# Kernel tuning notes

Hardware: AMD Instinct MI355X
Metric: run time of the kernel (lower is better)

The kernel has to match this reference:

```python
import jax, jax.numpy as jnp
import numpy as np

E = 16      # num experts
K = 2       # top-k
EPS = np.finfo(float).eps


def setup_inputs() -> dict:
    key = jax.random.key(0)
    k1, k2, k3 = jax.random.split(key, 3)
    B, D_IN, D_OUT = 16384, 1024, 512
    x = jax.random.normal(k1, (B, D_IN), dtype=jnp.float32)
    w_router = jax.random.normal(k2, (D_IN, E), dtype=jnp.float32) * 0.02
    w_experts = jax.random.normal(k3, (E, D_IN, D_OUT), dtype=jnp.float32) * 0.02
    return {"x": x, "w_router": w_router, "w_experts": w_experts}


def reference(x, w_router, w_experts):
    # --- noisy_top_k_gating (eval path: clean logits, no noise) ---
    logits = x @ w_router                      # [B, E]
    top_vals, top_idx = jax.lax.top_k(logits, K)   # [B, K]
    top_gates = jax.nn.softmax(top_vals, axis=1)   # softmax over top-k logits
    B = x.shape[0]
    gates = jnp.zeros_like(logits).at[jnp.arange(B)[:, None], top_idx].set(top_gates)  # [B, E]

    # --- per-expert encode (dense form; zero gates null out non-dispatched pairs,
    #     matching SparseDispatcher's sparse dispatch/combine math exactly) ---
    expert_out = jnp.einsum('bd,edh->beh', x, w_experts)  # [B, E, d_out]

    # --- SparseDispatcher.combine: exp -> gate-weight -> index_add -> eps clamp -> log ---
    combined = jnp.einsum('be,beh->bh', gates, jnp.exp(expert_out))  # [B, d_out]
    combined = jnp.where(combined == 0, jnp.asarray(EPS, combined.dtype), combined)
    return jnp.log(combined)
```

## Files before the change

### kernel.cpp

```cpp
#include <hip/hip_runtime.h>
#include <hip/hip_bf16.h>

typedef unsigned short u16_t;
typedef unsigned int   u32_t;

#define B_ROWS  16384
#define D_IN    1024
#define D_OUT   512
#define NEXP    16
#define CNT_STRIDE 16
#define EPSF    2.2204460492503131e-16f

using short8  = __attribute__((ext_vector_type(8))) short;
using floatx4 = __attribute__((ext_vector_type(4))) float;

__device__ __forceinline__ u16_t f2bf(float f) {
    u32_t u = __float_as_uint(f);
    u += 0x7fffu + ((u >> 16) & 1u);
    return (u16_t)(u >> 16);
}

__global__ __launch_bounds__(256) void transpose_wr(
        const float* __restrict__ wr, float* __restrict__ wrT) {
    int i = blockIdx.x * 256 + threadIdx.x;
    int e = i >> 10, d = i & 1023;
    wrT[i] = wr[d * NEXP + e];
}

__global__ __launch_bounds__(256) void convert_x(
        const float* __restrict__ x, u16_t* __restrict__ xb) {
    size_t i = ((size_t)blockIdx.x * 256 + threadIdx.x) * 8;
    float4 a = *(const float4*)(x + i);
    float4 b = *(const float4*)(x + i + 4);
    union { u16_t us[8]; uint4 v; } p;
    p.us[0] = f2bf(a.x); p.us[1] = f2bf(a.y); p.us[2] = f2bf(a.z); p.us[3] = f2bf(a.w);
    p.us[4] = f2bf(b.x); p.us[5] = f2bf(b.y); p.us[6] = f2bf(b.z); p.us[7] = f2bf(b.w);
    *(uint4*)(xb + i) = p.v;
}

__global__ __launch_bounds__(256) void convert_wT(
        const float* __restrict__ w, u16_t* __restrict__ wT) {
    int b = blockIdx.x;
    int e  = b >> 8;
    int k0 = ((b >> 1) & 127) * 8;
    int n  = (b & 1) * 256 + threadIdx.x;
    const float* src = w + ((size_t)e * D_IN + k0) * D_OUT + n;
    union { u16_t us[8]; uint4 v; } p;
    #pragma unroll
    for (int j = 0; j < 8; ++j) p.us[j] = f2bf(src[(size_t)j * D_OUT]);
    *(uint4*)(wT + ((size_t)e * D_OUT + n) * D_IN + k0) = p.v;
}

__global__ __launch_bounds__(256) void router_kernel(
        const float* __restrict__ x, const float* __restrict__ wrT,
        int* __restrict__ counts, int* __restrict__ rowlist,
        float* __restrict__ gatelist) {
    __shared__ float wsh[NEXP * D_IN];
    __shared__ int hist[NEXP], base[NEXP], hist2[NEXP];
    __shared__ unsigned char eidx_sh[32][2];
    __shared__ float g_sh[32][2];

    int t = threadIdx.x;
    {
        const float4* src = (const float4*)wrT;
        float4* dst = (float4*)wsh;
        #pragma unroll
        for (int i = 0; i < 16; ++i) dst[t + 256 * i] = src[t + 256 * i];
    }
    if (t < NEXP) { hist[t] = 0; hist2[t] = 0; }
    __syncthreads();

    int lr = t >> 3, q = t & 7;
    int row = blockIdx.x * 32 + lr;
    const float4* xq = (const float4*)(x + (size_t)row * D_IN + q * 128);

    double acc[NEXP];
    #pragma unroll
    for (int e = 0; e < NEXP; ++e) acc[e] = 0.0;

    for (int i = 0; i < 32; ++i) {
        int ii = (i + q * 4) & 31;
        float4 xv = xq[ii];
        double x0 = xv.x, x1 = xv.y, x2 = xv.z, x3 = xv.w;
        int d = q * 128 + ii * 4;
        #pragma unroll
        for (int e = 0; e < NEXP; ++e) {
            float4 wv = *(const float4*)(&wsh[e * D_IN + d]);
            acc[e] += x0 * (double)wv.x;
            acc[e] += x1 * (double)wv.y;
            acc[e] += x2 * (double)wv.z;
            acc[e] += x3 * (double)wv.w;
        }
    }
    #pragma unroll
    for (int e = 0; e < NEXP; ++e) {
        acc[e] += __shfl_xor(acc[e], 1);
        acc[e] += __shfl_xor(acc[e], 2);
        acc[e] += __shfl_xor(acc[e], 4);
    }
    if (q == 0) {
        int i1 = 0; double v1 = acc[0];
        #pragma unroll
        for (int e = 1; e < NEXP; ++e) if (acc[e] > v1) { v1 = acc[e]; i1 = e; }
        int i2 = -1; double v2 = -1.0e300;
        #pragma unroll
        for (int e = 0; e < NEXP; ++e) if (e != i1 && acc[e] > v2) { v2 = acc[e]; i2 = e; }
        double ed = exp(v2 - v1);
        double s = 1.0 + ed;
        eidx_sh[lr][0] = (unsigned char)i1; g_sh[lr][0] = (float)(1.0 / s);
        eidx_sh[lr][1] = (unsigned char)i2; g_sh[lr][1] = (float)(ed / s);
        atomicAdd(&hist[i1], 1);
        atomicAdd(&hist[i2], 1);
    }
    __syncthreads();
    if (t < NEXP) base[t] = atomicAdd(&counts[t * CNT_STRIDE], hist[t]);
    __syncthreads();
    if (t < 64) {
        int r = t >> 1, sl = t & 1;
        int e = eidx_sh[r][sl];
        int pos = base[e] + atomicAdd(&hist2[e], 1);
        rowlist[e * B_ROWS + pos] = ((blockIdx.x * 32 + r) << 1) | sl;
        gatelist[e * B_ROWS + pos] = g_sh[r][sl];
    }
}

template<bool USE_CONTRIB>
__global__ __launch_bounds__(256) void moe_gemm_bf16(
        const u16_t* __restrict__ xb, const u16_t* __restrict__ wT,
        const int* __restrict__ counts, const int* __restrict__ rowlist,
        const float* __restrict__ gatelist,
        float* __restrict__ out, float* __restrict__ contrib) {
    int e = blockIdx.z;
    int n_e = counts[e * CNT_STRIDE];
    int ty = blockIdx.y;
    if (ty * 128 >= n_e) return;
    int n0 = blockIdx.x * 128;

    __shared__ u16_t Ash[128][40];
    __shared__ u16_t Bsh[128][40];
    __shared__ int   rid_sh[128];
    __shared__ float gt_sh[128];

    int t = threadIdx.x;
    if (t < 128) {
        int gi = ty * 128 + t;
        int v = 0; float g = 0.f;
        if (gi < n_e) { v = rowlist[e * B_ROWS + gi]; g = gatelist[e * B_ROWS + gi]; }
        rid_sh[t] = v; gt_sh[t] = g;
    }
    __syncthreads();

    int hr = t >> 1, hh = t & 1;
    const u16_t* aptr = xb + (size_t)(rid_sh[hr] >> 1) * D_IN + hh * 16;
    const u16_t* bptr = wT + ((size_t)e * D_OUT + n0 + hr) * D_IN + hh * 16;

    int lane = t & 63, wv = t >> 6;
    int wm = wv >> 1, wn = wv & 1;
    int lm = lane & 15, q = lane >> 4;

    floatx4 acc[4][4];
    #pragma unroll
    for (int mi = 0; mi < 4; ++mi)
        #pragma unroll
        for (int ni = 0; ni < 4; ++ni)
            acc[mi][ni] = (floatx4){0.f, 0.f, 0.f, 0.f};

    for (int it = 0; it < D_IN / 32; ++it) {
        uint4 a0 = *(const uint4*)(aptr);
        uint4 a1 = *(const uint4*)(aptr + 8);
        uint4 b0 = *(const uint4*)(bptr);
        uint4 b1 = *(const uint4*)(bptr + 8);
        aptr += 32; bptr += 32;

        __syncthreads();
        *(uint4*)(&Ash[hr][hh * 16])     = a0;
        *(uint4*)(&Ash[hr][hh * 16 + 8]) = a1;
        *(uint4*)(&Bsh[hr][hh * 16])     = b0;
        *(uint4*)(&Bsh[hr][hh * 16 + 8]) = b1;
        __syncthreads();

        short8 afr[4];
        #pragma unroll
        for (int mi = 0; mi < 4; ++mi)
            afr[mi] = *(const short8*)(&Ash[wm * 64 + mi * 16 + lm][q * 8]);
        short8 bfr[4];
        #pragma unroll
        for (int ni = 0; ni < 4; ++ni)
            bfr[ni] = *(const short8*)(&Bsh[wn * 64 + ni * 16 + lm][q * 8]);
        #pragma unroll
        for (int mi = 0; mi < 4; ++mi)
            #pragma unroll
            for (int ni = 0; ni < 4; ++ni)
                acc[mi][ni] = __builtin_amdgcn_mfma_f32_16x16x32_bf16(
                    afr[mi], bfr[ni], acc[mi][ni], 0, 0, 0);
    }

    #pragma unroll
    for (int mi = 0; mi < 4; ++mi) {
        int rbase = wm * 64 + mi * 16 + q * 4;
        #pragma unroll
        for (int r = 0; r < 4; ++r) {
            int row = rbase + r;
            int gi = ty * 128 + row;
            bool ok = gi < n_e;
            int v = rid_sh[row];
            float g = gt_sh[row];
            size_t orow = (size_t)(v >> 1) * D_OUT;
            #pragma unroll
            for (int ni = 0; ni < 4; ++ni) {
                int c = n0 + wn * 64 + ni * 16 + lm;
                float val = g * __expf(acc[mi][ni][r]);
                if (ok) {
                    if (USE_CONTRIB) {
                        float* dst = (v & 1) ? contrib : out;
                        dst[orow + c] = val;
                    } else {
                        atomicAdd(&out[orow + c], val);
                    }
                }
            }
        }
    }
}

template<bool USE_CONTRIB>
__global__ __launch_bounds__(256) void moe_gemm(
        const float* __restrict__ x, const float* __restrict__ w,
        const int* __restrict__ counts, const int* __restrict__ rowlist,
        const float* __restrict__ gatelist,
        float* __restrict__ out, float* __restrict__ contrib) {
    int e = blockIdx.z;
    int n_e = counts[e * CNT_STRIDE];
    int ty = blockIdx.y;
    if (ty * 128 >= n_e) return;
    int n0 = blockIdx.x * 128;

    __shared__ u16_t Ash[128][40];
    __shared__ u32_t Bsh[16][132];
    __shared__ int   rid_sh[128];
    __shared__ float gt_sh[128];

    int t = threadIdx.x;
    if (t < 128) {
        int gi = ty * 128 + t;
        int v = 0; float g = 0.f;
        if (gi < n_e) { v = rowlist[e * B_ROWS + gi]; g = gatelist[e * B_ROWS + gi]; }
        rid_sh[t] = v; gt_sh[t] = g;
    }
    __syncthreads();

    int ar = t >> 1, ah = t & 1;
    const float* xptr = x + (size_t)(rid_sh[ar] >> 1) * D_IN + ah * 16;
    int bkp = t >> 4, bng = t & 15;
    const float* wptr = w + (size_t)e * (D_IN * D_OUT)
                          + (size_t)(2 * bkp) * D_OUT + n0 + bng * 8;

    int lane = t & 63, wv = t >> 6;
    int wm = wv >> 1, wn = wv & 1;
    int lm = lane & 15, q = lane >> 4;

    floatx4 acc[4][4];
    #pragma unroll
    for (int mi = 0; mi < 4; ++mi)
        #pragma unroll
        for (int ni = 0; ni < 4; ++ni)
            acc[mi][ni] = (floatx4){0.f, 0.f, 0.f, 0.f};

    for (int it = 0; it < D_IN / 32; ++it) {
        float4 av0 = *(const float4*)(xptr + 0);
        float4 av1 = *(const float4*)(xptr + 4);
        float4 av2 = *(const float4*)(xptr + 8);
        float4 av3 = *(const float4*)(xptr + 12);
        xptr += 32;
        float4 b0 = *(const float4*)(wptr + 0);
        float4 b1 = *(const float4*)(wptr + 4);
        float4 b2 = *(const float4*)(wptr + D_OUT);
        float4 b3 = *(const float4*)(wptr + D_OUT + 4);
        wptr += 32 * D_OUT;

        __syncthreads();
        {
            union { u16_t us[16]; uint4 v[2]; } ap;
            float af[16] = {av0.x, av0.y, av0.z, av0.w, av1.x, av1.y, av1.z, av1.w,
                            av2.x, av2.y, av2.z, av2.w, av3.x, av3.y, av3.z, av3.w};
            #pragma unroll
            for (int j = 0; j < 16; ++j) ap.us[j] = f2bf(af[j]);
            *(uint4*)(&Ash[ar][ah * 16])     = ap.v[0];
            *(uint4*)(&Ash[ar][ah * 16 + 8]) = ap.v[1];
        }
        {
            union { u32_t up[8]; uint4 v[2]; } bp;
            bp.up[0] = (u32_t)f2bf(b0.x) | ((u32_t)f2bf(b2.x) << 16);
            bp.up[1] = (u32_t)f2bf(b0.y) | ((u32_t)f2bf(b2.y) << 16);
            bp.up[2] = (u32_t)f2bf(b0.z) | ((u32_t)f2bf(b2.z) << 16);
            bp.up[3] = (u32_t)f2bf(b0.w) | ((u32_t)f2bf(b2.w) << 16);
            bp.up[4] = (u32_t)f2bf(b1.x) | ((u32_t)f2bf(b3.x) << 16);
            bp.up[5] = (u32_t)f2bf(b1.y) | ((u32_t)f2bf(b3.y) << 16);
            bp.up[6] = (u32_t)f2bf(b1.z) | ((u32_t)f2bf(b3.z) << 16);
            bp.up[7] = (u32_t)f2bf(b1.w) | ((u32_t)f2bf(b3.w) << 16);
            *(uint4*)(&Bsh[bkp][bng * 8])     = bp.v[0];
            *(uint4*)(&Bsh[bkp][bng * 8 + 4]) = bp.v[1];
        }
        __syncthreads();

        short8 afr[4];
        #pragma unroll
        for (int mi = 0; mi < 4; ++mi)
            afr[mi] = *(const short8*)(&Ash[wm * 64 + mi * 16 + lm][q * 8]);
        short8 bfr[4];
        #pragma unroll
        for (int ni = 0; ni < 4; ++ni) {
            int nn = wn * 64 + ni * 16 + lm;
            union { uint4 u; short8 s; } cv;
            cv.u.x = Bsh[q * 4 + 0][nn];
            cv.u.y = Bsh[q * 4 + 1][nn];
            cv.u.z = Bsh[q * 4 + 2][nn];
            cv.u.w = Bsh[q * 4 + 3][nn];
            bfr[ni] = cv.s;
        }
        #pragma unroll
        for (int mi = 0; mi < 4; ++mi)
            #pragma unroll
            for (int ni = 0; ni < 4; ++ni)
                acc[mi][ni] = __builtin_amdgcn_mfma_f32_16x16x32_bf16(
                    afr[mi], bfr[ni], acc[mi][ni], 0, 0, 0);
    }

    #pragma unroll
    for (int mi = 0; mi < 4; ++mi) {
        int rbase = wm * 64 + mi * 16 + q * 4;
        #pragma unroll
        for (int r = 0; r < 4; ++r) {
            int row = rbase + r;
            int gi = ty * 128 + row;
            bool ok = gi < n_e;
            int v = rid_sh[row];
            float g = gt_sh[row];
            size_t orow = (size_t)(v >> 1) * D_OUT;
            #pragma unroll
            for (int ni = 0; ni < 4; ++ni) {
                int c = n0 + wn * 64 + ni * 16 + lm;
                float val = g * __expf(acc[mi][ni][r]);
                if (ok) {
                    if (USE_CONTRIB) {
                        float* dst = (v & 1) ? contrib : out;
                        dst[orow + c] = val;
                    } else {
                        atomicAdd(&out[orow + c], val);
                    }
                }
            }
        }
    }
}

__global__ __launch_bounds__(256) void combine_add_log(
        float* __restrict__ out, const float* __restrict__ contrib, int n4) {
    int i = blockIdx.x * blockDim.x + threadIdx.x;
    if (i >= n4) return;
    float4 a = ((const float4*)out)[i];
    float4 b = ((const float4*)contrib)[i];
    float4 r;
    float s;
    s = a.x + b.x; s = (s == 0.f) ? EPSF : s; r.x = __logf(s);
    s = a.y + b.y; s = (s == 0.f) ? EPSF : s; r.y = __logf(s);
    s = a.z + b.z; s = (s == 0.f) ? EPSF : s; r.z = __logf(s);
    s = a.w + b.w; s = (s == 0.f) ? EPSF : s; r.w = __logf(s);
    ((float4*)out)[i] = r;
}

__global__ __launch_bounds__(256) void log_inplace(float* __restrict__ out, int n4) {
    int i = blockIdx.x * blockDim.x + threadIdx.x;
    if (i >= n4) return;
    float4 a = ((float4*)out)[i];
    float4 r;
    float s;
    s = a.x; s = (s == 0.f) ? EPSF : s; r.x = __logf(s);
    s = a.y; s = (s == 0.f) ? EPSF : s; r.y = __logf(s);
    s = a.z; s = (s == 0.f) ? EPSF : s; r.z = __logf(s);
    s = a.w; s = (s == 0.f) ? EPSF : s; r.w = __logf(s);
    ((float4*)out)[i] = r;
}

extern "C" void kernel_launch(void* const* d_in, const int* in_sizes, int n_in,
                              void* d_out, int out_size, void* d_ws, size_t ws_size,
                              hipStream_t stream) {
    const float* x  = (const float*)d_in[0];
    const float* wr = (const float*)d_in[1];
    const float* we = (const float*)d_in[2];
    float* out = (float*)d_out;
    char* ws = (char*)d_ws;

    size_t off = 0;
    int*   counts  = (int*)(ws + off);   off += 1024;
    int*   rowlist = (int*)(ws + off);   off += (size_t)NEXP * B_ROWS * 4;
    float* gates   = (float*)(ws + off); off += (size_t)NEXP * B_ROWS * 4;
    float* wrT     = (float*)(ws + off); off += (size_t)NEXP * D_IN * 4;
    float* contrib = (float*)(ws + off); off += (size_t)B_ROWS * D_OUT * 4;
    size_t tier2_need = off;
    u16_t* xb      = (u16_t*)(ws + off); off += (size_t)B_ROWS * D_IN * 2;
    u16_t* wTb     = (u16_t*)(ws + off); off += (size_t)NEXP * D_IN * D_OUT * 2;
    size_t tier3_need = off;

    hipMemsetAsync(counts, 0, 1024, stream);
    transpose_wr<<<NEXP * D_IN / 256, 256, 0, stream>>>(wr, wrT);
    router_kernel<<<B_ROWS / 32, 256, 0, stream>>>(x, wrT, counts, rowlist, gates);

    dim3 g(D_OUT / 128, B_ROWS / 128, NEXP);
    int n4 = B_ROWS * D_OUT / 4;

    if (ws_size >= tier3_need) {
        convert_x<<<(B_ROWS * D_IN / 8) / 256, 256, 0, stream>>>(x, xb);
        convert_wT<<<NEXP * 128 * 2, 256, 0, stream>>>(we, wTb);
        moe_gemm_bf16<true><<<g, 256, 0, stream>>>(xb, wTb, counts, rowlist, gates, out, contrib);
        combine_add_log<<<(n4 + 255) / 256, 256, 0, stream>>>(out, contrib, n4);
    } else if (ws_size >= tier2_need) {
        moe_gemm<true><<<g, 256, 0, stream>>>(x, we, counts, rowlist, gates, out, contrib);
        combine_add_log<<<(n4 + 255) / 256, 256, 0, stream>>>(out, contrib, n4);
    } else {
        hipMemsetAsync(out, 0, (size_t)B_ROWS * D_OUT * 4, stream);
        moe_gemm<false><<<g, 256, 0, stream>>>(x, we, counts, rowlist, gates, out, nullptr);
        log_inplace<<<(n4 + 255) / 256, 256, 0, stream>>>(out, n4);
    }
}
```

Baseline: 272.4 us.

## Fuse prep kernels, convert x in router, use direct-to-LDS loads with swizzle

Result: slower. 301.4 us (+10.7%).

```diff
diff --git a/kernel.cpp b/kernel.cpp
--- a/kernel.cpp
+++ b/kernel.cpp
@@ -1,5 +1,6 @@
 #include <hip/hip_runtime.h>
 #include <hip/hip_bf16.h>
+#include <stdint.h>
 
 typedef unsigned short u16_t;
 typedef unsigned int   u32_t;
@@ -20,41 +21,40 @@
     return (u16_t)(u >> 16);
 }
 
-__global__ __launch_bounds__(256) void transpose_wr(
-        const float* __restrict__ wr, float* __restrict__ wrT) {
-    int i = blockIdx.x * 256 + threadIdx.x;
-    int e = i >> 10, d = i & 1023;
-    wrT[i] = wr[d * NEXP + e];
-}
-
-__global__ __launch_bounds__(256) void convert_x(
-        const float* __restrict__ x, u16_t* __restrict__ xb) {
-    size_t i = ((size_t)blockIdx.x * 256 + threadIdx.x) * 8;
-    float4 a = *(const float4*)(x + i);
-    float4 b = *(const float4*)(x + i + 4);
-    union { u16_t us[8]; uint4 v; } p;
-    p.us[0] = f2bf(a.x); p.us[1] = f2bf(a.y); p.us[2] = f2bf(a.z); p.us[3] = f2bf(a.w);
-    p.us[4] = f2bf(b.x); p.us[5] = f2bf(b.y); p.us[6] = f2bf(b.z); p.us[7] = f2bf(b.w);
-    *(uint4*)(xb + i) = p.v;
-}
-
-__global__ __launch_bounds__(256) void convert_wT(
-        const float* __restrict__ w, u16_t* __restrict__ wT) {
-    int b = blockIdx.x;
-    int e  = b >> 8;
-    int k0 = ((b >> 1) & 127) * 8;
-    int n  = (b & 1) * 256 + threadIdx.x;
-    const float* src = w + ((size_t)e * D_IN + k0) * D_OUT + n;
-    union { u16_t us[8]; uint4 v; } p;
-    #pragma unroll
-    for (int j = 0; j < 8; ++j) p.us[j] = f2bf(src[(size_t)j * D_OUT]);
-    *(uint4*)(wT + ((size_t)e * D_OUT + n) * D_IN + k0) = p.v;
+__device__ __forceinline__ void gload_lds16(const void* g, void* l) {
+    __builtin_amdgcn_global_load_lds(
+        (const __attribute__((address_space(1))) void*)g,
+        (__attribute__((address_space(3))) void*)l, 16, 0, 0);
+}
+
+__global__ __launch_bounds__(256) void prep_kernel(
+        const float* __restrict__ wr, float* __restrict__ wrT,
+        const float* __restrict__ we, u16_t* __restrict__ wT,
+        int* __restrict__ counts) {
+    int b = blockIdx.x, t = threadIdx.x;
+    if (b < 64) {
+        int i = b * 256 + t;
+        int e = i >> 10, d = i & 1023;
+        wrT[i] = wr[d * NEXP + e];
+    } else if (b == 64) {
+        counts[t] = 0;
+    } else {
+        int bb = b - 65;
+        int e  = bb >> 8;
+        int k0 = ((bb >> 1) & 127) * 8;
+        int n  = (bb & 1) * 256 + t;
+        const float* src = we + ((size_t)e * D_IN + k0) * D_OUT + n;
+        union { u16_t us[8]; uint4 v; } p;
+        #pragma unroll
+        for (int j = 0; j < 8; ++j) p.us[j] = f2bf(src[(size_t)j * D_OUT]);
+        *(uint4*)(wT + ((size_t)e * D_OUT + n) * D_IN + k0) = p.v;
+    }
 }
 
 __global__ __launch_bounds__(256) void router_kernel(
         const float* __restrict__ x, const float* __restrict__ wrT,
         int* __restrict__ counts, int* __restrict__ rowlist,
-        float* __restrict__ gatelist) {
+        float* __restrict__ gatelist, u16_t* __restrict__ xb) {
     __shared__ float wsh[NEXP * D_IN];
     __shared__ int hist[NEXP], base[NEXP], hist2[NEXP];
     __shared__ unsigned char eidx_sh[32][2];
@@ -79,8 +79,14 @@
     for (int e = 0; e < NEXP; ++e) acc[e] = 0.0;
 
     for (int i = 0; i < 32; ++i) {
-        int ii = (i + q * 4) & 31;
+        int ii = (i + q) & 31;
         float4 xv = xq[ii];
+        if (xb) {
+            uint2 pk;
+            pk.x = (u32_t)f2bf(xv.x) | ((u32_t)f2bf(xv.y) << 16);
+            pk.y = (u32_t)f2bf(xv.z) | ((u32_t)f2bf(xv.w) << 16);
+            *(uint2*)(xb + (size_t)row * D_IN + q * 128 + ii * 4) = pk;
+        }
         double x0 = xv.x, x1 = xv.y, x2 = xv.z, x3 = xv.w;
         int d = q * 128 + ii * 4;
         #pragma unroll
@@ -130,14 +136,17 @@
         const int* __restrict__ counts, const int* __restrict__ rowlist,
         const float* __restrict__ gatelist,
         float* __restrict__ out, float* __restrict__ contrib) {
-    int e = blockIdx.z;
+    int bid = blockIdx.x;
+    int s   = bid >> 3;
+    int e   = ((bid & 7) << 1) | (s >> 9);
+    s &= 511;
+    int tx = s & 3, ty = s >> 2;
     int n_e = counts[e * CNT_STRIDE];
-    int ty = blockIdx.y;
     if (ty * 128 >= n_e) return;
-    int n0 = blockIdx.x * 128;
-
-    __shared__ u16_t Ash[128][40];
-    __shared__ u16_t Bsh[128][40];
+    int n0 = tx * 128;
+
+    __shared__ u16_t Ash[128 * 64];
+    __shared__ u16_t Bsh[128 * 64];
     __shared__ int   rid_sh[128];
     __shared__ float gt_sh[128];
 
@@ -150,13 +159,22 @@
     }
     __syncthreads();
 
-    int hr = t >> 1, hh = t & 1;
-    const u16_t* aptr = xb + (size_t)(rid_sh[hr] >> 1) * D_IN + hh * 16;
-    const u16_t* bptr = wT + ((size_t)e * D_OUT + n0 + hr) * D_IN + hh * 16;
-
     int lane = t & 63, wv = t >> 6;
+
+    const u16_t* asrc[4];
+    const u16_t* bsrc[4];
+    #pragma unroll
+    for (int r = 0; r < 4; ++r) {
+        int i   = r * 256 + wv * 64 + lane;
+        int row = i >> 3;
+        int ss  = (i & 7) ^ (row & 7);
+        asrc[r] = xb + (size_t)(rid_sh[row] >> 1) * D_IN + ss * 8;
+        bsrc[r] = wT + ((size_t)e * D_OUT + n0 + row) * D_IN + ss * 8;
+    }
+
     int wm = wv >> 1, wn = wv & 1;
     int lm = lane & 15, q = lane >> 4;
+    int l7 = lm & 7;
 
     floatx4 acc[4][4];
     #pragma unroll
@@ -165,34 +183,32 @@
         for (int ni = 0; ni < 4; ++ni)
             acc[mi][ni] = (floatx4){0.f, 0.f, 0.f, 0.f};
 
-    for (int it = 0; it < D_IN / 32; ++it) {
-        uint4 a0 = *(const uint4*)(aptr);
-        uint4 a1 = *(const uint4*)(aptr + 8);
-        uint4 b0 = *(const uint4*)(bptr);
-        uint4 b1 = *(const uint4*)(bptr + 8);
-        aptr += 32; bptr += 32;
-
+    for (int it = 0; it < D_IN / 64; ++it) {
+        if (it) __syncthreads();
+        #pragma unroll
+        for (int r = 0; r < 4; ++r) {
+            gload_lds16(asrc[r], (char*)Ash + r * 4096 + wv * 1024);
+            gload_lds16(bsrc[r], (char*)Bsh + r * 4096 + wv * 1024);
+            asrc[r] += 64; bsrc[r] += 64;
+        }
         __syncthreads();
-        *(uint4*)(&Ash[hr][hh * 16])     = a0;
-        *(uint4*)(&Ash[hr][hh * 16 + 8]) = a1;
-        *(uint4*)(&Bsh[hr][hh * 16])     = b0;
-        *(uint4*)(&Bsh[hr][hh * 16 + 8]) = b1;
-        __syncthreads();
-
-        short8 afr[4];
-        #pragma unroll
-        for (int mi = 0; mi < 4; ++mi)
-            afr[mi] = *(const short8*)(&Ash[wm * 64 + mi * 16 + lm][q * 8]);
-        short8 bfr[4];
-        #pragma unroll
-        for (int ni = 0; ni < 4; ++ni)
-            bfr[ni] = *(const short8*)(&Bsh[wn * 64 + ni * 16 + lm][q * 8]);
-        #pragma unroll
-        for (int mi = 0; mi < 4; ++mi)
-            #pragma unroll
-            for (int ni = 0; ni < 4; ++ni)
-                acc[mi][ni] = __builtin_amdgcn_mfma_f32_16x16x32_bf16(
-                    afr[mi], bfr[ni], acc[mi][ni], 0, 0, 0);
+
+        #pragma unroll
+        for (int kk = 0; kk < 2; ++kk) {
+            int sw = ((((kk << 2) | q) ^ l7) << 3);
+            short8 afr[4], bfr[4];
+            #pragma unroll
+            for (int f = 0; f < 4; ++f) {
+                afr[f] = *(const short8*)(Ash + ((wm * 64 + f * 16 + lm) << 6) + sw);
+                bfr[f] = *(const short8*)(Bsh + ((wn * 64 + f * 16 + lm) << 6) + sw);
+            }
+            #pragma unroll
+            for (int mi = 0; mi < 4; ++mi)
+                #pragma unroll
+                for (int ni = 0; ni < 4; ++ni)
+                    acc[mi][ni] = __builtin_amdgcn_mfma_f32_16x16x32_bf16(
+                        afr[mi], bfr[ni], acc[mi][ni], 0, 0, 0);
+        }
     }
 
     #pragma unroll
@@ -402,22 +418,26 @@
     u16_t* wTb     = (u16_t*)(ws + off); off += (size_t)NEXP * D_IN * D_OUT * 2;
     size_t tier3_need = off;
 
-    hipMemsetAsync(counts, 0, 1024, stream);
-    transpose_wr<<<NEXP * D_IN / 256, 256, 0, stream>>>(wr, wrT);
-    router_kernel<<<B_ROWS / 32, 256, 0, stream>>>(x, wrT, counts, rowlist, gates);
-
-    dim3 g(D_OUT / 128, B_ROWS / 128, NEXP);
+    bool tier3 = ws_size >= tier3_need;
+    bool tier2 = ws_size >= tier2_need;
+
+    prep_kernel<<<tier3 ? (65 + NEXP * 256) : 65, 256, 0, stream>>>(
+        wr, wrT, we, wTb, counts);
+    router_kernel<<<B_ROWS / 32, 256, 0, stream>>>(
+        x, wrT, counts, rowlist, gates, tier3 ? xb : (u16_t*)nullptr);
+
     int n4 = B_ROWS * D_OUT / 4;
 
-    if (ws_size >= tier3_need) {
-        convert_x<<<(B_ROWS * D_IN / 8) / 256, 256, 0, stream>>>(x, xb);
-        convert_wT<<<NEXP * 128 * 2, 256, 0, stream>>>(we, wTb);
-        moe_gemm_bf16<true><<<g, 256, 0, stream>>>(xb, wTb, counts, rowlist, gates, out, contrib);
+    if (tier3) {
+        moe_gemm_bf16<true><<<8192, 256, 0, stream>>>(
+            xb, wTb, counts, rowlist, gates, out, contrib);
         combine_add_log<<<(n4 + 255) / 256, 256, 0, stream>>>(out, contrib, n4);
-    } else if (ws_size >= tier2_need) {
+    } else if (tier2) {
+        dim3 g(D_OUT / 128, B_ROWS / 128, NEXP);
         moe_gemm<true><<<g, 256, 0, stream>>>(x, we, counts, rowlist, gates, out, contrib);
         combine_add_log<<<(n4 + 255) / 256, 256, 0, stream>>>(out, contrib, n4);
     } else {
+        dim3 g(D_OUT / 128, B_ROWS / 128, NEXP);
         hipMemsetAsync(out, 0, (size_t)B_ROWS * D_OUT * 4, stream);
         moe_gemm<false><<<g, 256, 0, stream>>>(x, we, counts, rowlist, gates, out, nullptr);
         log_inplace<<<(n4 + 255) / 256, 256, 0, stream>>>(out, n4);
```
